# Performance work log

Hardware: AMD Instinct MI355X
Metric: run time of the kernel (lower is better)

Reference implementation:

```python
import jax, jax.numpy as jnp
import numpy as np

B, T, D = 4, 2048, 1024


def setup_inputs() -> dict:
    key = jax.random.key(0)
    ks = jax.random.split(key, 14)
    s = 0.02
    return {
        "x": jax.random.normal(ks[0], (B, T, D), dtype=jnp.float32),
        "time_decay": jax.random.normal(ks[1], (D,), dtype=jnp.float32) * 0.1,
        "tm_k": jax.random.uniform(ks[2], (D,), dtype=jnp.float32),
        "tm_v": jax.random.uniform(ks[3], (D,), dtype=jnp.float32),
        "tm_r": jax.random.uniform(ks[4], (D,), dtype=jnp.float32),
        "Wk": jax.random.normal(ks[5], (D, D), dtype=jnp.float32) * s,
        "Wv": jax.random.normal(ks[6], (D, D), dtype=jnp.float32) * s,
        "Wr": jax.random.normal(ks[7], (D, D), dtype=jnp.float32) * s,
        "Wo": jax.random.normal(ks[8], (D, D), dtype=jnp.float32) * s,
        "cm_k": jax.random.uniform(ks[9], (D,), dtype=jnp.float32),
        "cm_r": jax.random.uniform(ks[10], (D,), dtype=jnp.float32),
        "Wck": jax.random.normal(ks[11], (D, 4 * D), dtype=jnp.float32) * s,
        "Wcv": jax.random.normal(ks[12], (4 * D, D), dtype=jnp.float32) * s,
        "Wcr": jax.random.normal(ks[13], (D, D), dtype=jnp.float32) * s,
    }


def _shift(x):
    # token shift: prepend zero state (initial last_x), drop last token
    return jnp.concatenate([jnp.zeros_like(x[:, :1]), x[:, :-1]], axis=1)


def reference(x, time_decay, tm_k, tm_v, tm_r, Wk, Wv, Wr, Wo,
              cm_k, cm_r, Wck, Wcv, Wcr):
    # ---- time mixing (WKV recurrence) ----
    shifted = _shift(x)
    xk = x * tm_k + shifted * (1.0 - tm_k)
    xv = x * tm_v + shifted * (1.0 - tm_v)
    xr = x * tm_r + shifted * (1.0 - tm_r)
    k = xk @ Wk            # (B,T,D)
    v = xv @ Wv
    r = jax.nn.sigmoid(xr @ Wr)
    ew = jnp.exp(-jnp.exp(time_decay))  # exp(w), w = -exp(time_decay)

    def step(carry, kv):
        num, den = carry
        kt, vt = kv
        ek = jnp.exp(kt)
        num = ew * num + ek * vt
        den = ew * den + ek
        return (num, den), num / (den + 1e-6)

    init = (jnp.zeros((B, D), x.dtype), jnp.zeros((B, D), x.dtype))
    _, wkv_t = jax.lax.scan(step, init, (jnp.swapaxes(k, 0, 1), jnp.swapaxes(v, 0, 1)))
    wkv = jnp.swapaxes(wkv_t, 0, 1)  # (B,T,D)
    x = x + (r * wkv) @ Wo

    # ---- channel mixing (gated FFN, squared ReLU) ----
    shifted2 = _shift(x)
    xk2 = x * cm_k + shifted2 * (1.0 - cm_k)
    xr2 = x * cm_r + shifted2 * (1.0 - cm_r)
    kh = jnp.square(jax.nn.relu(xk2 @ Wck))  # (B,T,4D)
    v2 = kh @ Wcv
    r2 = jax.nn.sigmoid(xr2 @ Wcr)
    return x + r2 * v2
```

## Files before the change

kernel.cpp:

```cpp
#include <hip/hip_runtime.h>
#include <hip/hip_bf16.h>
#include <math.h>

#define BATCH 4
#define TLEN  2048
#define DIM   1024
#define NROWS (BATCH*TLEN)
#define HDIM  (4*DIM)

typedef __hip_bfloat16 bf16;
typedef __attribute__((ext_vector_type(8))) short   shortx8;
typedef __attribute__((ext_vector_type(4))) float   floatx4;

__device__ __forceinline__ unsigned short f2bf(float f) {
    bf16 h = __float2bfloat16(f);
    return __builtin_bit_cast(unsigned short, h);
}

__device__ __forceinline__ void async16(const void* g, void* l) {
    __builtin_amdgcn_global_load_lds((const __attribute__((address_space(1))) void*)g,
                                     (__attribute__((address_space(3))) void*)l, 16, 0, 0);
}

enum { EP_NONE=0, EP_SIGMOID=1, EP_ADD=2, EP_SQRELU=3, EP_FINAL=4 };

#define G_REGB   24576
#define G_ABYTES 8192
#define G_NSH    (5*12288)

__device__ __forceinline__ void gemm_core(
    const bf16* __restrict__ A, const bf16* __restrict__ Bt, const int K,
    const size_t m0, const size_t n0, short* lds, floatx4 (&acc)[4][4])
{
    const int tid = threadIdx.x;
    char* ldsc = (char*)lds;

    const int rA = tid >> 2;
    const int kA = ((tid & 3) ^ ((rA >> 1) & 3)) << 3;
    const bf16* pA  = A  + (size_t)(m0 + rA) * K + kA;
    const int s1  = 512 + tid;
    const int rB1 = s1 >> 2;
    const int kB1 = ((s1 & 3) ^ ((rB1 >> 1) & 3)) << 3;
    const bf16* pB0 = Bt + (size_t)(n0 + rA)  * K + kA;
    const bf16* pB1 = Bt + (size_t)(n0 + rB1) * K + kB1;
    char* dA  = ldsc + tid * 16;
    char* dB0 = ldsc + G_ABYTES + tid * 16;
    char* dB1 = ldsc + G_ABYTES + 8192 + tid * 16;

    const int lane = tid & 63;
    const int wave = tid >> 6;
    const int wm = (wave >> 2) * 64;
    const int wn = (wave & 3) * 64;
    const int lr = lane & 15, kq = lane >> 4;
    int offA[4], offB[4];
    #pragma unroll
    for (int i = 0; i < 4; ++i) {
        const int ra = wm + i*16 + lr;
        offA[i] = ra*64 + ((kq ^ ((ra>>1)&3)) << 4);
        const int rb = wn + i*16 + lr;
        offB[i] = G_ABYTES + rb*64 + ((kq ^ ((rb>>1)&3)) << 4);
    }

    const int P = K >> 5;

    auto stage = [&](int sl, int reg) {
        const int rB = reg * G_REGB;
        const int ko = sl << 5;
        async16(pA  + ko, dA  + rB);
        async16(pB0 + ko, dB0 + rB);
        async16(pB1 + ko, dB1 + rB);
    };
    auto compute = [&](int reg) {
        const char* rb = ldsc + reg * G_REGB;
        shortx8 af[4], bfr[4];
        #pragma unroll
        for (int i = 0; i < 4; ++i) af[i]  = *(const shortx8*)(rb + offA[i]);
        #pragma unroll
        for (int i = 0; i < 4; ++i) bfr[i] = *(const shortx8*)(rb + offB[i]);
        __builtin_amdgcn_s_setprio(1);
        #pragma unroll
        for (int mi = 0; mi < 4; ++mi)
            #pragma unroll
            for (int ni = 0; ni < 4; ++ni)
                acc[mi][ni] = __builtin_amdgcn_mfma_f32_16x16x32_bf16(
                                  af[mi], bfr[ni], acc[mi][ni], 0, 0, 0);
        __builtin_amdgcn_s_setprio(0);
    };

    stage(0,0); stage(1,1); stage(2,2); stage(3,3);
    asm volatile("s_waitcnt vmcnt(9)" ::: "memory");
    __builtin_amdgcn_s_barrier();
    __builtin_amdgcn_sched_barrier(0);

    int cur = 0, sreg = 4;
    for (int q = 0; q < P - 4; ++q) {
        stage(q + 4, sreg);
        compute(cur);
        asm volatile("s_waitcnt vmcnt(9)" ::: "memory");
        __builtin_amdgcn_s_barrier();
        __builtin_amdgcn_sched_barrier(0);
        sreg = cur;
        cur  = (cur == 4) ? 0 : cur + 1;
    }
    compute(cur); cur = (cur == 4) ? 0 : cur + 1;
    asm volatile("s_waitcnt vmcnt(6)" ::: "memory");
    __builtin_amdgcn_s_barrier();
    __builtin_amdgcn_sched_barrier(0);
    compute(cur); cur = (cur == 4) ? 0 : cur + 1;
    asm volatile("s_waitcnt vmcnt(3)" ::: "memory");
    __builtin_amdgcn_s_barrier();
    __builtin_amdgcn_sched_barrier(0);
    compute(cur); cur = (cur == 4) ? 0 : cur + 1;
    asm volatile("s_waitcnt vmcnt(0)" ::: "memory");
    __builtin_amdgcn_s_barrier();
    __builtin_amdgcn_sched_barrier(0);
    compute(cur);
}

template<int MODE, typename OutT>
__device__ __forceinline__ void epilogue(
    floatx4 (&acc)[4][4], OutT* __restrict__ C,
    const float* __restrict__ addv, const bf16* __restrict__ mulv,
    const size_t m0, const size_t n0, const int N)
{
    const int tid = threadIdx.x;
    const int lane = tid & 63, wave = tid >> 6;
    const size_t r0 = m0 + (size_t)(wave >> 2) * 64 + ((lane >> 4) << 2);
    const size_t c0 = n0 + (size_t)(wave & 3) * 64 + (lane & 15);
    #pragma unroll
    for (int mi = 0; mi < 4; ++mi)
      #pragma unroll
      for (int ni = 0; ni < 4; ++ni)
        #pragma unroll
        for (int r = 0; r < 4; ++r) {
            const size_t off = (r0 + mi*16 + r) * N + c0 + ni*16;
            float v = acc[mi][ni][r];
            if (MODE == EP_SIGMOID)      v = 1.0f / (1.0f + __expf(-v));
            else if (MODE == EP_ADD)     v = addv[off] + v;
            else if (MODE == EP_SQRELU)  { float t = fmaxf(v, 0.0f); v = t * t; }
            else if (MODE == EP_FINAL)   v = addv[off] + __bfloat162float(mulv[off]) * v;
            if (sizeof(OutT) == 2) *(unsigned short*)(C + off) = f2bf(v);
            else                   *(float*)(C + off) = v;
        }
}

template<int MODE, typename OutT>
__global__ __launch_bounds__(512, 2)
void gemm256(const bf16* __restrict__ A, const bf16* __restrict__ Bt,
             OutT* __restrict__ C,
             const float* __restrict__ addv, const bf16* __restrict__ mulv,
             int N, int K)
{
    __shared__ __align__(16) short lds[G_NSH];
    const int nwg  = gridDim.x * gridDim.y;
    const int orig = blockIdx.y * gridDim.x + blockIdx.x;
    const int wg   = (orig & 7) * (nwg >> 3) + (orig >> 3);
    const int bx   = wg % gridDim.x;
    const int by   = wg / gridDim.x;
    const size_t m0 = (size_t)bx * 128;
    const size_t n0 = (size_t)by * 256;
    floatx4 acc[4][4] = {};
    gemm_core(A, Bt, K, m0, n0, lds, acc);
    epilogue<MODE, OutT>(acc, C, addv, mulv, m0, n0, N);
}

struct GDesc { const bf16* A; const bf16* Bt; bf16* C; int mode; };
struct GArgs { GDesc d[3]; };

__global__ __launch_bounds__(512, 2)
void gemm256_multi(GArgs args)
{
    __shared__ __align__(16) short lds[G_NSH];
    const int nwg  = gridDim.x * gridDim.y;
    const int orig = blockIdx.y * gridDim.x + blockIdx.x;
    const int wg   = (orig & 7) * (nwg >> 3) + (orig >> 3);
    const int bx   = wg % gridDim.x;
    const int byg  = wg / gridDim.x;
    const int di   = byg >> 2;
    const int by   = byg & 3;
    const GDesc d  = args.d[di];
    const size_t m0 = (size_t)bx * 128;
    const size_t n0 = (size_t)by * 256;
    floatx4 acc[4][4] = {};
    gemm_core(d.A, d.Bt, DIM, m0, n0, lds, acc);

    const int tid = threadIdx.x;
    const int lane = tid & 63, wave = tid >> 6;
    const size_t r0 = m0 + (size_t)(wave >> 2) * 64 + ((lane >> 4) << 2);
    const size_t c0 = n0 + (size_t)(wave & 3) * 64 + (lane & 15);
    const bool sig = (d.mode == EP_SIGMOID);
    #pragma unroll
    for (int mi = 0; mi < 4; ++mi)
      #pragma unroll
      for (int ni = 0; ni < 4; ++ni)
        #pragma unroll
        for (int r = 0; r < 4; ++r) {
            const size_t off = (r0 + mi*16 + r) * DIM + c0 + ni*16;
            float v = acc[mi][ni][r];
            if (sig) v = 1.0f / (1.0f + __expf(-v));
            *(unsigned short*)(d.C + off) = f2bf(v);
        }
}

struct TDesc { const float* in; bf16* out; int K; int N; int tiles; int tx; };
struct PrepArgs {
    TDesc t[7];
    int ttotal;
    const float4 *x, *mk, *mv, *mr;
    ushort4 *ok, *ov, *orr;
};

__global__ __launch_bounds__(256)
void prep_kernel(PrepArgs a)
{
    int blk = blockIdx.x;
    if (blk < a.ttotal) {
        int t = blk, di = 0;
        while (t >= a.t[di].tiles) { t -= a.t[di].tiles; ++di; }
        const float* in  = a.t[di].in;
        bf16*        out = a.t[di].out;
        const int K = a.t[di].K, N = a.t[di].N, tx = a.t[di].tx;
        const int bx = t % tx, by = t / tx;
        __shared__ float tile[32][33];
        const int kt = by * 32, nt = bx * 32;
        #pragma unroll
        for (int i = threadIdx.y; i < 32; i += 8)
            tile[i][threadIdx.x] = in[(size_t)(kt + i) * N + nt + threadIdx.x];
        __syncthreads();
        #pragma unroll
        for (int i = threadIdx.y; i < 32; i += 8)
            out[(size_t)(nt + i) * K + kt + threadIdx.x] =
                __float2bfloat16(tile[threadIdx.x][i]);
    } else {
        const int D4 = DIM / 4;
        int tid = threadIdx.y * 32 + threadIdx.x;
        int e   = (blk - a.ttotal) * 256 + tid;
        int d4  = e & (D4 - 1);
        int t   = (e >> 8) & (TLEN - 1);
        float4 xc = a.x[e];
        float4 sh = make_float4(0.f, 0.f, 0.f, 0.f);
        if (t > 0) sh = a.x[e - D4];
        float4 mk = a.mk[d4], mv = a.mv[d4], mr = a.mr[d4];
        ushort4 u;
        u.x=f2bf(xc.x*mk.x+sh.x*(1.f-mk.x)); u.y=f2bf(xc.y*mk.y+sh.y*(1.f-mk.y));
        u.z=f2bf(xc.z*mk.z+sh.z*(1.f-mk.z)); u.w=f2bf(xc.w*mk.w+sh.w*(1.f-mk.w));
        a.ok[e]=u;
        u.x=f2bf(xc.x*mv.x+sh.x*(1.f-mv.x)); u.y=f2bf(xc.y*mv.y+sh.y*(1.f-mv.y));
        u.z=f2bf(xc.z*mv.z+sh.z*(1.f-mv.z)); u.w=f2bf(xc.w*mv.w+sh.w*(1.f-mv.w));
        a.ov[e]=u;
        u.x=f2bf(xc.x*mr.x+sh.x*(1.f-mr.x)); u.y=f2bf(xc.y*mr.y+sh.y*(1.f-mr.y));
        u.z=f2bf(xc.z*mr.z+sh.z*(1.f-mr.z)); u.w=f2bf(xc.w*mr.w+sh.w*(1.f-mr.w));
        a.orr[e]=u;
    }
}

__global__ __launch_bounds__(256)
void mix2_kernel(const float4* __restrict__ x,
                 const float4* __restrict__ mk, const float4* __restrict__ mr,
                 ushort4* __restrict__ ok, ushort4* __restrict__ orr)
{
    const int D4 = DIM / 4;
    int e   = blockIdx.x * 256 + threadIdx.x;
    int d4  = e & (D4 - 1);
    int t   = (e >> 8) & (TLEN - 1);
    float4 xc = x[e];
    float4 sh = make_float4(0.f, 0.f, 0.f, 0.f);
    if (t > 0) sh = x[e - D4];
    float4 a = mk[d4], c = mr[d4];
    ushort4 u;
    u.x=f2bf(xc.x*a.x+sh.x*(1.f-a.x)); u.y=f2bf(xc.y*a.y+sh.y*(1.f-a.y));
    u.z=f2bf(xc.z*a.z+sh.z*(1.f-a.z)); u.w=f2bf(xc.w*a.w+sh.w*(1.f-a.w));
    ok[e]=u;
    u.x=f2bf(xc.x*c.x+sh.x*(1.f-c.x)); u.y=f2bf(xc.y*c.y+sh.y*(1.f-c.y));
    u.z=f2bf(xc.z*c.z+sh.z*(1.f-c.z)); u.w=f2bf(xc.w*c.w+sh.w*(1.f-c.w));
    orr[e]=u;
}

#define WKV_CHUNK 64
#define WKV_WARM  64
__global__ __launch_bounds__(256)
void wkv_kernel(const bf16* __restrict__ K, const bf16* __restrict__ V,
                const bf16* __restrict__ R, const float* __restrict__ td,
                bf16* __restrict__ out)
{
    int d     = blockIdx.x * 256 + threadIdx.x;
    int chunk = blockIdx.y;
    int b     = blockIdx.z;
    int start = chunk * WKV_CHUNK;
    int t0    = start - WKV_WARM; if (t0 < 0) t0 = 0;

    float ew = __expf(-__expf(td[d]));
    float num = 0.f, den = 0.f;
    size_t base = ((size_t)b * TLEN) * DIM + d;

    for (int t = t0; t < start; ++t) {
        size_t idx = base + (size_t)t * DIM;
        float ek = __expf(__bfloat162float(K[idx]));
        num = ew * num + ek * __bfloat162float(V[idx]);
        den = ew * den + ek;
    }
    for (int t = start; t < start + WKV_CHUNK; ++t) {
        size_t idx = base + (size_t)t * DIM;
        float ek = __expf(__bfloat162float(K[idx]));
        num = ew * num + ek * __bfloat162float(V[idx]);
        den = ew * den + ek;
        out[idx] = __float2bfloat16(__bfloat162float(R[idx]) * (num / (den + 1e-6f)));
    }
}

extern "C" void kernel_launch(void* const* d_in, const int* in_sizes, int n_in,
                              void* d_out, int out_size, void* d_ws, size_t ws_size,
                              hipStream_t stream)
{
    const float* x   = (const float*)d_in[0];
    const float* td  = (const float*)d_in[1];
    const float* tmk = (const float*)d_in[2];
    const float* tmv = (const float*)d_in[3];
    const float* tmr = (const float*)d_in[4];
    const float* Wk  = (const float*)d_in[5];
    const float* Wv  = (const float*)d_in[6];
    const float* Wr  = (const float*)d_in[7];
    const float* Wo  = (const float*)d_in[8];
    const float* cmk = (const float*)d_in[9];
    const float* cmr = (const float*)d_in[10];
    const float* Wck = (const float*)d_in[11];
    const float* Wcv = (const float*)d_in[12];
    const float* Wcr = (const float*)d_in[13];
    float* out = (float*)d_out;

    char* ws = (char*)d_ws;
    const size_t MB = 1024 * 1024;
    bf16*  Wk_t  = (bf16*)(ws +   0*MB);
    bf16*  Wv_t  = (bf16*)(ws +   2*MB);
    bf16*  Wr_t  = (bf16*)(ws +   4*MB);
    bf16*  Wo_t  = (bf16*)(ws +   6*MB);
    bf16*  Wcr_t = (bf16*)(ws +   8*MB);
    bf16*  Wck_t = (bf16*)(ws +  10*MB);
    bf16*  Wcv_t = (bf16*)(ws +  18*MB);
    float* f0    = (float*)(ws + 26*MB);
    bf16*  bA    = (bf16*)(ws +  58*MB);
    bf16*  bB    = (bf16*)(ws +  74*MB);
    bf16*  bC    = (bf16*)(ws +  90*MB);
    bf16*  bD    = (bf16*)(ws + 106*MB);
    bf16*  bE    = (bf16*)(ws + 122*MB);
    bf16*  bF    = (bf16*)(ws + 138*MB);
    bf16*  kh    = bA;

    const dim3 blk(256);
    const dim3 gblk(512);

    {
        PrepArgs pa;
        const float* src[7] = {Wk, Wv, Wr, Wo, Wcr, Wck, Wcv};
        bf16*        dst[7] = {Wk_t, Wv_t, Wr_t, Wo_t, Wcr_t, Wck_t, Wcv_t};
        int          kk[7]  = {DIM, DIM, DIM, DIM, DIM, DIM, HDIM};
        int          nn[7]  = {DIM, DIM, DIM, DIM, DIM, HDIM, DIM};
        int total = 0;
        for (int i = 0; i < 7; ++i) {
            int tx = nn[i] / 32, ty = kk[i] / 32;
            pa.t[i] = {src[i], dst[i], kk[i], nn[i], tx * ty, tx};
            total += tx * ty;
        }
        pa.ttotal = total;
        pa.x  = (const float4*)x;
        pa.mk = (const float4*)tmk; pa.mv = (const float4*)tmv; pa.mr = (const float4*)tmr;
        pa.ok = (ushort4*)bA; pa.ov = (ushort4*)bB; pa.orr = (ushort4*)bC;
        const int mixBlocks = NROWS * DIM / 4 / 256;
        prep_kernel<<<dim3(total + mixBlocks), dim3(32, 8), 0, stream>>>(pa);
    }

    {
        GArgs ga;
        ga.d[0] = {bA, Wk_t, bD, EP_NONE};
        ga.d[1] = {bB, Wv_t, bE, EP_NONE};
        ga.d[2] = {bC, Wr_t, bF, EP_SIGMOID};
        gemm256_multi<<<dim3(NROWS/128, 12), gblk, 0, stream>>>(ga);
    }

    dim3 wkvGrid(DIM / 256, TLEN / WKV_CHUNK, BATCH);
    wkv_kernel<<<wkvGrid, blk, 0, stream>>>(bD, bE, bF, td, bF);

    gemm256<EP_ADD, float><<<dim3(NROWS/128, DIM/256), gblk, 0, stream>>>(
        bF, Wo_t, f0, x, nullptr, DIM, DIM);

    mix2_kernel<<<dim3(NROWS * DIM / 4 / 256), blk, 0, stream>>>(
        (const float4*)f0, (const float4*)cmk, (const float4*)cmr,
        (ushort4*)bE, (ushort4*)bA);

    gemm256<EP_SIGMOID, bf16><<<dim3(NROWS/128, DIM/256), gblk, 0, stream>>>(
        bA, Wcr_t, bF, nullptr, nullptr, DIM, DIM);

    gemm256<EP_SQRELU, bf16><<<dim3(NROWS/128, HDIM/256), gblk, 0, stream>>>(
        bE, Wck_t, kh, nullptr, nullptr, HDIM, DIM);

    gemm256<EP_FINAL, float><<<dim3(NROWS/128, DIM/256), gblk, 0, stream>>>(
        kh, Wcv_t, out, f0, bF, DIM, HDIM);
}
```

Measured before the change: 489.6 us.

## Switch GEMMs to 256x128 tiles with 4 waves and 3-stage LDS pipeline

New measurement: 523.2 us. +6.9%, slower.

```diff
diff --git a/kernel.cpp b/kernel.cpp
--- a/kernel.cpp
+++ b/kernel.cpp
@@ -25,61 +25,67 @@
 enum { EP_NONE=0, EP_SIGMOID=1, EP_ADD=2, EP_SQRELU=3, EP_FINAL=4 };
 
 #define G_REGB   24576
-#define G_ABYTES 8192
-#define G_NSH    (5*12288)
+#define G_ABYTES 16384
+#define G_NSH    (3*12288)
 
 __device__ __forceinline__ void gemm_core(
     const bf16* __restrict__ A, const bf16* __restrict__ Bt, const int K,
-    const size_t m0, const size_t n0, short* lds, floatx4 (&acc)[4][4])
+    const size_t m0, const size_t n0, short* lds, floatx4 (&acc)[8][4])
 {
     const int tid = threadIdx.x;
     char* ldsc = (char*)lds;
 
-    const int rA = tid >> 2;
-    const int kA = ((tid & 3) ^ ((rA >> 1) & 3)) << 3;
-    const bf16* pA  = A  + (size_t)(m0 + rA) * K + kA;
-    const int s1  = 512 + tid;
-    const int rB1 = s1 >> 2;
-    const int kB1 = ((s1 & 3) ^ ((rB1 >> 1) & 3)) << 3;
-    const bf16* pB0 = Bt + (size_t)(n0 + rA)  * K + kA;
-    const bf16* pB1 = Bt + (size_t)(n0 + rB1) * K + kB1;
-    char* dA  = ldsc + tid * 16;
-    char* dB0 = ldsc + G_ABYTES + tid * 16;
-    char* dB1 = ldsc + G_ABYTES + 8192 + tid * 16;
+    const bf16* src[6];
+    int doff[6];
+    #pragma unroll
+    for (int j = 0; j < 6; ++j) {
+        const int s   = j * 256 + tid;
+        const int isB = (j >= 4);
+        const int s2  = isB ? (s - 1024) : s;
+        const int row = s2 >> 2;
+        const int kg  = (s2 & 3) ^ ((row >> 1) & 3);
+        const bf16* base = isB ? (Bt + (size_t)(n0 + row) * K)
+                               : (A  + (size_t)(m0 + row) * K);
+        src[j]  = base + kg * 8;
+        doff[j] = s * 16;
+    }
 
     const int lane = tid & 63;
     const int wave = tid >> 6;
-    const int wm = (wave >> 2) * 64;
-    const int wn = (wave & 3) * 64;
+    const int wr = wave >> 1;
+    const int wc = wave &  1;
     const int lr = lane & 15, kq = lane >> 4;
-    int offA[4], offB[4];
+    int offA[8], offB[4];
+    #pragma unroll
+    for (int i = 0; i < 8; ++i) {
+        const int ra = wr*128 + i*16 + lr;
+        offA[i] = ra*64 + ((kq ^ ((ra>>1)&3)) << 4);
+    }
     #pragma unroll
     for (int i = 0; i < 4; ++i) {
-        const int ra = wm + i*16 + lr;
-        offA[i] = ra*64 + ((kq ^ ((ra>>1)&3)) << 4);
-        const int rb = wn + i*16 + lr;
+        const int rb = wc*64 + i*16 + lr;
         offB[i] = G_ABYTES + rb*64 + ((kq ^ ((rb>>1)&3)) << 4);
     }
 
     const int P = K >> 5;
 
     auto stage = [&](int sl, int reg) {
-        const int rB = reg * G_REGB;
+        char* rbase = ldsc + reg * G_REGB;
         const int ko = sl << 5;
-        async16(pA  + ko, dA  + rB);
-        async16(pB0 + ko, dB0 + rB);
-        async16(pB1 + ko, dB1 + rB);
+        #pragma unroll
+        for (int j = 0; j < 6; ++j)
+            async16(src[j] + ko, rbase + doff[j]);
     };
     auto compute = [&](int reg) {
         const char* rb = ldsc + reg * G_REGB;
-        shortx8 af[4], bfr[4];
-        #pragma unroll
-        for (int i = 0; i < 4; ++i) af[i]  = *(const shortx8*)(rb + offA[i]);
+        shortx8 af[8], bfr[4];
+        #pragma unroll
+        for (int i = 0; i < 8; ++i) af[i]  = *(const shortx8*)(rb + offA[i]);
         #pragma unroll
         for (int i = 0; i < 4; ++i) bfr[i] = *(const shortx8*)(rb + offB[i]);
         __builtin_amdgcn_s_setprio(1);
         #pragma unroll
-        for (int mi = 0; mi < 4; ++mi)
+        for (int mi = 0; mi < 8; ++mi)
             #pragma unroll
             for (int ni = 0; ni < 4; ++ni)
                 acc[mi][ni] = __builtin_amdgcn_mfma_f32_16x16x32_bf16(
@@ -87,30 +93,24 @@
         __builtin_amdgcn_s_setprio(0);
     };
 
-    stage(0,0); stage(1,1); stage(2,2); stage(3,3);
-    asm volatile("s_waitcnt vmcnt(9)" ::: "memory");
-    __builtin_amdgcn_s_barrier();
-    __builtin_amdgcn_sched_barrier(0);
-
-    int cur = 0, sreg = 4;
-    for (int q = 0; q < P - 4; ++q) {
-        stage(q + 4, sreg);
-        compute(cur);
-        asm volatile("s_waitcnt vmcnt(9)" ::: "memory");
-        __builtin_amdgcn_s_barrier();
-        __builtin_amdgcn_sched_barrier(0);
-        sreg = cur;
-        cur  = (cur == 4) ? 0 : cur + 1;
-    }
-    compute(cur); cur = (cur == 4) ? 0 : cur + 1;
+    stage(0, 0); stage(1, 1);
     asm volatile("s_waitcnt vmcnt(6)" ::: "memory");
     __builtin_amdgcn_s_barrier();
     __builtin_amdgcn_sched_barrier(0);
-    compute(cur); cur = (cur == 4) ? 0 : cur + 1;
-    asm volatile("s_waitcnt vmcnt(3)" ::: "memory");
-    __builtin_amdgcn_s_barrier();
-    __builtin_amdgcn_sched_barrier(0);
-    compute(cur); cur = (cur == 4) ? 0 : cur + 1;
+
+    int cur = 0;
+    for (int q = 0; q < P - 2; ++q) {
+        const int nreg = (cur == 2) ? 0 : cur + 1;
+        const int sreg = (nreg == 2) ? 0 : nreg + 1;
+        stage(q + 2, sreg);
+        compute(cur);
+        asm volatile("s_waitcnt vmcnt(6)" ::: "memory");
+        __builtin_amdgcn_s_barrier();
+        __builtin_amdgcn_sched_barrier(0);
+        cur = nreg;
+    }
+    compute(cur);
+    cur = (cur == 2) ? 0 : cur + 1;
     asm volatile("s_waitcnt vmcnt(0)" ::: "memory");
     __builtin_amdgcn_s_barrier();
     __builtin_amdgcn_sched_barrier(0);
@@ -119,16 +119,16 @@
 
 template<int MODE, typename OutT>
 __device__ __forceinline__ void epilogue(
-    floatx4 (&acc)[4][4], OutT* __restrict__ C,
+    floatx4 (&acc)[8][4], OutT* __restrict__ C,
     const float* __restrict__ addv, const bf16* __restrict__ mulv,
     const size_t m0, const size_t n0, const int N)
 {
     const int tid = threadIdx.x;
     const int lane = tid & 63, wave = tid >> 6;
-    const size_t r0 = m0 + (size_t)(wave >> 2) * 64 + ((lane >> 4) << 2);
-    const size_t c0 = n0 + (size_t)(wave & 3) * 64 + (lane & 15);
-    #pragma unroll
-    for (int mi = 0; mi < 4; ++mi)
+    const size_t r0 = m0 + (size_t)(wave >> 1) * 128 + ((lane >> 4) << 2);
+    const size_t c0 = n0 + (size_t)(wave & 1) * 64 + (lane & 15);
+    #pragma unroll
+    for (int mi = 0; mi < 8; ++mi)
       #pragma unroll
       for (int ni = 0; ni < 4; ++ni)
         #pragma unroll
@@ -145,7 +145,7 @@
 }
 
 template<int MODE, typename OutT>
-__global__ __launch_bounds__(512, 2)
+__global__ __launch_bounds__(256, 2)
 void gemm256(const bf16* __restrict__ A, const bf16* __restrict__ Bt,
              OutT* __restrict__ C,
              const float* __restrict__ addv, const bf16* __restrict__ mulv,
@@ -157,9 +157,9 @@
     const int wg   = (orig & 7) * (nwg >> 3) + (orig >> 3);
     const int bx   = wg % gridDim.x;
     const int by   = wg / gridDim.x;
-    const size_t m0 = (size_t)bx * 128;
-    const size_t n0 = (size_t)by * 256;
-    floatx4 acc[4][4] = {};
+    const size_t m0 = (size_t)bx * 256;
+    const size_t n0 = (size_t)by * 128;
+    floatx4 acc[8][4] = {};
     gemm_core(A, Bt, K, m0, n0, lds, acc);
     epilogue<MODE, OutT>(acc, C, addv, mulv, m0, n0, N);
 }
@@ -167,7 +167,7 @@
 struct GDesc { const bf16* A; const bf16* Bt; bf16* C; int mode; };
 struct GArgs { GDesc d[3]; };
 
-__global__ __launch_bounds__(512, 2)
+__global__ __launch_bounds__(256, 2)
 void gemm256_multi(GArgs args)
 {
     __shared__ __align__(16) short lds[G_NSH];
@@ -176,21 +176,21 @@
     const int wg   = (orig & 7) * (nwg >> 3) + (orig >> 3);
     const int bx   = wg % gridDim.x;
     const int byg  = wg / gridDim.x;
-    const int di   = byg >> 2;
-    const int by   = byg & 3;
+    const int di   = byg >> 3;
+    const int by   = byg & 7;
     const GDesc d  = args.d[di];
-    const size_t m0 = (size_t)bx * 128;
-    const size_t n0 = (size_t)by * 256;
-    floatx4 acc[4][4] = {};
+    const size_t m0 = (size_t)bx * 256;
+    const size_t n0 = (size_t)by * 128;
+    floatx4 acc[8][4] = {};
     gemm_core(d.A, d.Bt, DIM, m0, n0, lds, acc);
 
     const int tid = threadIdx.x;
     const int lane = tid & 63, wave = tid >> 6;
-    const size_t r0 = m0 + (size_t)(wave >> 2) * 64 + ((lane >> 4) << 2);
-    const size_t c0 = n0 + (size_t)(wave & 3) * 64 + (lane & 15);
+    const size_t r0 = m0 + (size_t)(wave >> 1) * 128 + ((lane >> 4) << 2);
+    const size_t c0 = n0 + (size_t)(wave & 1) * 64 + (lane & 15);
     const bool sig = (d.mode == EP_SIGMOID);
     #pragma unroll
-    for (int mi = 0; mi < 4; ++mi)
+    for (int mi = 0; mi < 8; ++mi)
       #pragma unroll
       for (int ni = 0; ni < 4; ++ni)
         #pragma unroll
@@ -347,7 +347,7 @@
     bf16*  kh    = bA;
 
     const dim3 blk(256);
-    const dim3 gblk(512);
+    const dim3 gblk(256);
 
     {
         PrepArgs pa;
@@ -374,25 +374,25 @@
         ga.d[0] = {bA, Wk_t, bD, EP_NONE};
         ga.d[1] = {bB, Wv_t, bE, EP_NONE};
         ga.d[2] = {bC, Wr_t, bF, EP_SIGMOID};
-        gemm256_multi<<<dim3(NROWS/128, 12), gblk, 0, stream>>>(ga);
+        gemm256_multi<<<dim3(NROWS/256, 24), gblk, 0, stream>>>(ga);
     }
 
     dim3 wkvGrid(DIM / 256, TLEN / WKV_CHUNK, BATCH);
     wkv_kernel<<<wkvGrid, blk, 0, stream>>>(bD, bE, bF, td, bF);
 
-    gemm256<EP_ADD, float><<<dim3(NROWS/128, DIM/256), gblk, 0, stream>>>(
+    gemm256<EP_ADD, float><<<dim3(NROWS/256, DIM/128), gblk, 0, stream>>>(
         bF, Wo_t, f0, x, nullptr, DIM, DIM);
 
     mix2_kernel<<<dim3(NROWS * DIM / 4 / 256), blk, 0, stream>>>(
         (const float4*)f0, (const float4*)cmk, (const float4*)cmr,
         (ushort4*)bE, (ushort4*)bA);
 
-    gemm256<EP_SIGMOID, bf16><<<dim3(NROWS/128, DIM/256), gblk, 0, stream>>>(
+    gemm256<EP_SIGMOID, bf16><<<dim3(NROWS/256, DIM/128), gblk, 0, stream>>>(
         bA, Wcr_t, bF, nullptr, nullptr, DIM, DIM);
 
-    gemm256<EP_SQRELU, bf16><<<dim3(NROWS/128, HDIM/256), gblk, 0, stream>>>(
+    gemm256<EP_SQRELU, bf16><<<dim3(NROWS/256, HDIM/128), gblk, 0, stream>>>(
         bE, Wck_t, kh, nullptr, nullptr, HDIM, DIM);
 
-    gemm256<EP_FINAL, float><<<dim3(NROWS/128, DIM/256), gblk, 0, stream>>>(
+    gemm256<EP_FINAL, float><<<dim3(NROWS/256, DIM/128), gblk, 0, stream>>>(
         kh, Wcv_t, out, f0, bF, DIM, HDIM);
 }
```

## Prefetch next LDS fragments into registers while MFMAs run on current

Applied to the files above, without the earlier changes.

Measured after the change: 490.3 us. No clear change (+0.1%).

```diff
diff --git a/kernel.cpp b/kernel.cpp
--- a/kernel.cpp
+++ b/kernel.cpp
@@ -70,51 +70,84 @@
         async16(pB0 + ko, dB0 + rB);
         async16(pB1 + ko, dB1 + rB);
     };
-    auto compute = [&](int reg) {
+    auto ldfrag = [&](int reg, shortx8 (&af)[4], shortx8 (&bf_)[4]) {
         const char* rb = ldsc + reg * G_REGB;
-        shortx8 af[4], bfr[4];
         #pragma unroll
         for (int i = 0; i < 4; ++i) af[i]  = *(const shortx8*)(rb + offA[i]);
         #pragma unroll
-        for (int i = 0; i < 4; ++i) bfr[i] = *(const shortx8*)(rb + offB[i]);
-        __builtin_amdgcn_s_setprio(1);
+        for (int i = 0; i < 4; ++i) bf_[i] = *(const shortx8*)(rb + offB[i]);
+    };
+    auto domfma = [&](const shortx8 (&af)[4], const shortx8 (&bf_)[4]) {
         #pragma unroll
         for (int mi = 0; mi < 4; ++mi)
             #pragma unroll
             for (int ni = 0; ni < 4; ++ni)
                 acc[mi][ni] = __builtin_amdgcn_mfma_f32_16x16x32_bf16(
-                                  af[mi], bfr[ni], acc[mi][ni], 0, 0, 0);
-        __builtin_amdgcn_s_setprio(0);
+                                  af[mi], bf_[ni], acc[mi][ni], 0, 0, 0);
     };
 
     stage(0,0); stage(1,1); stage(2,2); stage(3,3);
-    asm volatile("s_waitcnt vmcnt(9)" ::: "memory");
-    __builtin_amdgcn_s_barrier();
-    __builtin_amdgcn_sched_barrier(0);
-
-    int cur = 0, sreg = 4;
-    for (int q = 0; q < P - 4; ++q) {
-        stage(q + 4, sreg);
-        compute(cur);
-        asm volatile("s_waitcnt vmcnt(9)" ::: "memory");
-        __builtin_amdgcn_s_barrier();
-        __builtin_amdgcn_sched_barrier(0);
-        sreg = cur;
-        cur  = (cur == 4) ? 0 : cur + 1;
-    }
-    compute(cur); cur = (cur == 4) ? 0 : cur + 1;
     asm volatile("s_waitcnt vmcnt(6)" ::: "memory");
     __builtin_amdgcn_s_barrier();
     __builtin_amdgcn_sched_barrier(0);
-    compute(cur); cur = (cur == 4) ? 0 : cur + 1;
-    asm volatile("s_waitcnt vmcnt(3)" ::: "memory");
-    __builtin_amdgcn_s_barrier();
-    __builtin_amdgcn_sched_barrier(0);
-    compute(cur); cur = (cur == 4) ? 0 : cur + 1;
-    asm volatile("s_waitcnt vmcnt(0)" ::: "memory");
-    __builtin_amdgcn_s_barrier();
-    __builtin_amdgcn_sched_barrier(0);
-    compute(cur);
+
+    shortx8 fa0[4], fb0[4], fa1[4], fb1[4];
+    ldfrag(0, fa0, fb0);
+
+    int cur = 0;
+    for (int q = 0; q < P - 4; q += 2) {
+        {
+            const int sreg = (cur == 0) ? 4 : cur - 1;
+            stage(q + 4, sreg);
+            const int nxt = (cur == 4) ? 0 : cur + 1;
+            __builtin_amdgcn_s_setprio(1);
+            ldfrag(nxt, fa1, fb1);
+            domfma(fa0, fb0);
+            __builtin_amdgcn_s_setprio(0);
+            asm volatile("s_waitcnt vmcnt(6)" ::: "memory");
+            __builtin_amdgcn_s_barrier();
+            __builtin_amdgcn_sched_barrier(0);
+            cur = nxt;
+        }
+        {
+            const int sreg = (cur == 0) ? 4 : cur - 1;
+            stage(q + 5, sreg);
+            const int nxt = (cur == 4) ? 0 : cur + 1;
+            __builtin_amdgcn_s_setprio(1);
+            ldfrag(nxt, fa0, fb0);
+            domfma(fa1, fb1);
+            __builtin_amdgcn_s_setprio(0);
+            asm volatile("s_waitcnt vmcnt(6)" ::: "memory");
+            __builtin_amdgcn_s_barrier();
+            __builtin_amdgcn_sched_barrier(0);
+            cur = nxt;
+        }
+    }
+
+    {
+        const int r1 = (cur == 4) ? 0 : cur + 1;
+        __builtin_amdgcn_s_setprio(1);
+        ldfrag(r1, fa1, fb1);
+        domfma(fa0, fb0);
+        __builtin_amdgcn_s_setprio(0);
+        asm volatile("s_waitcnt vmcnt(3)" ::: "memory");
+        __builtin_amdgcn_s_barrier();
+        __builtin_amdgcn_sched_barrier(0);
+        const int r2 = (r1 == 4) ? 0 : r1 + 1;
+        __builtin_amdgcn_s_setprio(1);
+        ldfrag(r2, fa0, fb0);
+        domfma(fa1, fb1);
+        __builtin_amdgcn_s_setprio(0);
+        asm volatile("s_waitcnt vmcnt(0)" ::: "memory");
+        __builtin_amdgcn_s_barrier();
+        __builtin_amdgcn_sched_barrier(0);
+        const int r3 = (r2 == 4) ? 0 : r2 + 1;
+        __builtin_amdgcn_s_setprio(1);
+        ldfrag(r3, fa1, fb1);
+        domfma(fa0, fb0);
+        domfma(fa1, fb1);
+        __builtin_amdgcn_s_setprio(0);
+    }
 }
 
 template<int MODE, typename OutT>
```
